# Optimization experiments

Measured on AMD Instinct MI355X. Metric: run time of the kernel, lower is better.

The kernel has to match this reference:

```python
import jax, jax.numpy as jnp
import numpy as np

NUM_HEADS = 8
CHUNK = 2
TAU = 2.0

# --- LIF neuron with ATan surrogate gradient (spikingjelly MultiStepLIFNode, hard reset to 0, detach_reset) ---
@jax.custom_vjp
def spike(x):
    return (x >= 0.0).astype(x.dtype)

def _spike_fwd(x):
    return spike(x), x

def _spike_bwd(x, g):
    alpha = 2.0
    sg = (alpha / 2.0) / (1.0 + (jnp.pi / 2.0 * alpha * x) ** 2)
    return (g * sg,)

spike.defvjp(_spike_fwd, _spike_bwd)

def lif(x_seq, v_th=1.0):
    # x_seq: [T, ...]; v' = v + (x - v)/tau ; spike if v' >= v_th ; hard reset v=0 (reset path detached)
    def step(v, x):
        v = v + (x - v) / TAU
        s = spike(v - v_th)
        v = v * (1.0 - jax.lax.stop_gradient(s))
        return v, s
    _, s = jax.lax.scan(step, jnp.zeros_like(x_seq[0]), x_seq)
    return s

def conv1x1_bn(x, W, scale, bias, conv_bias=None):
    # 1x1 conv over channel dim + eval-mode BN (per-channel affine)
    y = jnp.einsum('tbchw,dc->tbdhw', x, W)
    if conv_bias is not None:
        y = y + conv_bias[None, None, :, None, None]
    return y * scale[None, None, :, None, None] + bias[None, None, :, None, None]


def setup_inputs() -> dict:
    key = jax.random.key(0)
    ks = jax.random.split(key, 16)
    T, B, C, H, W = 4, 32, 512, 16, 16
    s = 1.0 / np.sqrt(C)
    return {
        'x': jax.random.normal(ks[0], (T, B, C, H, W), jnp.float32),
        'Wq': jax.random.normal(ks[1], (C, C), jnp.float32) * s,
        'q_scale': jax.random.uniform(ks[2], (C,), jnp.float32, 0.5, 1.5),
        'q_bias': jax.random.normal(ks[3], (C,), jnp.float32) * 0.1,
        'Wk': jax.random.normal(ks[4], (C, C), jnp.float32) * s,
        'k_scale': jax.random.uniform(ks[5], (C,), jnp.float32, 0.5, 1.5),
        'k_bias': jax.random.normal(ks[6], (C,), jnp.float32) * 0.1,
        'Wv': jax.random.normal(ks[7], (C, C), jnp.float32) * s,
        'v_scale': jax.random.uniform(ks[8], (C,), jnp.float32, 0.5, 1.5),
        'v_bias': jax.random.normal(ks[9], (C,), jnp.float32) * 0.1,
        'Wp': jax.random.normal(ks[10], (C, C), jnp.float32) * s,
        'bp': jax.random.normal(ks[11], (C,), jnp.float32) * 0.1,
        'p_scale': jax.random.uniform(ks[12], (C,), jnp.float32, 0.5, 1.5),
        'p_bias': jax.random.normal(ks[13], (C,), jnp.float32) * 0.1,
    }


def reference(x, Wq, q_scale, q_bias, Wk, k_scale, k_bias, Wv, v_scale, v_bias, Wp, bp, p_scale, p_bias):
    T, B, C, H, W = x.shape
    N = H * W
    hd = C // NUM_HEADS
    identity = x

    xs = lif(x)  # shortcut_lif

    def qkv_branch(W_, sc, bi):
        y = lif(conv1x1_bn(xs, W_, sc, bi))           # [T,B,C,H,W] spikes
        # flatten(3).transpose(-1,-2).reshape(...heads...).permute == split C, swap N/hd
        return jnp.swapaxes(y.reshape(T, B, NUM_HEADS, hd, N), -1, -2)  # [T,B,h,N,hd]

    q = qkv_branch(Wq, q_scale, q_bias)
    k = qkv_branch(Wk, k_scale, k_bias)
    v = qkv_branch(Wv, v_scale, v_bias)

    # STAtten: temporal chunking, linear attention q @ (k^T v)
    scaling = 1.0 / H
    nc = T // CHUNK

    def to_chunks(y):  # [T,B,h,N,hd] -> [nc,B,h,CHUNK*N,hd]
        return (y.reshape(nc, CHUNK, B, NUM_HEADS, N, hd)
                 .transpose(0, 2, 3, 1, 4, 5)
                 .reshape(nc, B, NUM_HEADS, CHUNK * N, hd))

    qc, kc, vc = to_chunks(q), to_chunks(k), to_chunks(v)
    attn = jnp.einsum('nbhsd,nbhse->nbhde', kc, vc) * scaling   # [nc,B,h,hd,hd]
    out = jnp.einsum('nbhsd,nbhde->nbhse', qc, attn)            # [nc,B,h,CHUNK*N,hd]
    out = (out.reshape(nc, B, NUM_HEADS, CHUNK, N, hd)
              .transpose(0, 3, 1, 2, 4, 5)
              .reshape(T, B, NUM_HEADS, N, hd))

    x2 = jnp.swapaxes(out, -1, -2).reshape(T, B, C, N)          # [T,B,C,N]
    x2 = lif(x2, v_th=0.5).reshape(T, B, C, H, W)               # attn_lif

    x3 = conv1x1_bn(x2, Wp, p_scale, p_bias, conv_bias=bp)      # proj conv+BN
    return x3 + identity, v
```

## Files before the change

### kernel.cpp

```cpp
#include <hip/hip_runtime.h>

typedef unsigned short ushort_t;
typedef unsigned char u8;
typedef short bf16x8 __attribute__((ext_vector_type(8)));
typedef float f32x4 __attribute__((ext_vector_type(4)));

#define T_DIM 4
#define B_DIM 32
#define C_DIM 512
#define N_DIM 256

__device__ __forceinline__ float bf2f(ushort_t u) {
  union { unsigned int i; float f; } x;
  x.i = ((unsigned int)u) << 16;
  return x.f;
}
__device__ __forceinline__ ushort_t f2bf(float f) {
  unsigned int u = __float_as_uint(f);
  u = (u + 0x7FFFu + ((u >> 16) & 1u)) >> 16;
  return (ushort_t)u;
}

__device__ __forceinline__ void gload16(const void* g, void* l) {
  __builtin_amdgcn_global_load_lds(
      (const __attribute__((address_space(1))) unsigned int*)g,
      (__attribute__((address_space(3))) unsigned int*)l, 16, 0, 0);
}

__device__ __forceinline__ unsigned int spike2bf(unsigned int w) {
  unsigned int r;
  asm("v_mul_u32_u24 %0, 0x3f80, %1" : "=v"(r) : "v"(w));
  return r;
}
__device__ __forceinline__ bf16x8 expand_spikes(uint2 raw) {
  union { bf16x8 v; unsigned int u[4]; } bu;
  bu.u[0] = spike2bf(__builtin_amdgcn_perm(0u, raw.x, 0x05010400u));
  bu.u[1] = spike2bf(__builtin_amdgcn_perm(0u, raw.x, 0x07030602u));
  bu.u[2] = spike2bf(__builtin_amdgcn_perm(0u, raw.y, 0x05010400u));
  bu.u[3] = spike2bf(__builtin_amdgcn_perm(0u, raw.y, 0x07030602u));
  return bu.v;
}

__global__ __launch_bounds__(256) void k0_split(
    const float* __restrict__ Wq, const float* __restrict__ Wk,
    const float* __restrict__ Wv, const float* __restrict__ Wp,
    ushort_t* __restrict__ Sqkv, ushort_t* __restrict__ Sp)
{
  int gid = blockIdx.x * 256 + threadIdx.x;
  int w = gid >> 15;
  int off = (gid & 32767) * 8;
  const float* src = (w == 0) ? Wq : ((w == 1) ? Wk : ((w == 2) ? Wv : Wp));
  ushort_t* dst = (w < 3) ? (Sqkv + (size_t)w * 3 * 262144) : Sp;
  float wv[8];
  *(float4*)&wv[0] = *(const float4*)(src + off);
  *(float4*)&wv[4] = *(const float4*)(src + off + 4);
  ushort_t hi[8], mi[8], lo[8];
#pragma unroll
  for (int i = 0; i < 8; i++) {
    float f = wv[i];
    ushort_t h = f2bf(f);  float r  = f - bf2f(h);
    ushort_t m = f2bf(r);  float r2 = r - bf2f(m);
    ushort_t l = f2bf(r2);
    hi[i] = h; mi[i] = m; lo[i] = l;
  }
  *(uint4*)(dst + off)              = *(uint4*)&hi[0];
  *(uint4*)(dst + 262144 + off)     = *(uint4*)&mi[0];
  *(uint4*)(dst + 2 * 262144 + off) = *(uint4*)&lo[0];
}

__global__ __launch_bounds__(256) void k1_shortcut_lif(
    const float* __restrict__ x, u8* __restrict__ xsT8)
{
  const int n0 = blockIdx.x * 64;
  const int c0 = blockIdx.y * 64;
  const int b  = blockIdx.z;
  __shared__ u8 sm[64][80];
  const int tid = threadIdx.x;
  const int r  = tid >> 2;
  const int j0 = (tid & 3) * 16;
  float v[16];
#pragma unroll
  for (int i = 0; i < 16; i++) v[i] = 0.f;
  for (int t = 0; t < T_DIM; t++) {
    const float* xp = x + ((((size_t)t * B_DIM + b) * C_DIM) + c0 + r) * N_DIM + n0 + j0;
    float xv[16];
    *(float4*)&xv[0]  = *(const float4*)xp;
    *(float4*)&xv[4]  = *(const float4*)(xp + 4);
    *(float4*)&xv[8]  = *(const float4*)(xp + 8);
    *(float4*)&xv[12] = *(const float4*)(xp + 12);
    __syncthreads();
#pragma unroll
    for (int i = 0; i < 16; i++) {
      float nv = v[i] + (xv[i] - v[i]) * 0.5f;
      bool s = (nv >= 1.0f);
      v[i] = s ? 0.f : nv;
      sm[j0 + i][r] = s ? (u8)1 : (u8)0;
    }
    __syncthreads();
    union { uint4 u; u8 b[16]; } ov;
#pragma unroll
    for (int i = 0; i < 16; i++) ov.b[i] = sm[r][j0 + i];
    u8* op = xsT8 + ((((size_t)t * B_DIM + b) * N_DIM) + n0 + r) * C_DIM + c0 + j0;
    *(uint4*)op = ov.u;
  }
}

__global__ __launch_bounds__(512, 4) void k2_qkv(
    const u8* __restrict__ xsT8, const ushort_t* __restrict__ Sqkv,
    const float* __restrict__ qsc, const float* __restrict__ qbi,
    const float* __restrict__ ksc, const float* __restrict__ kbi,
    const float* __restrict__ vsc, const float* __restrict__ vbi,
    u8* __restrict__ qs8T, u8* __restrict__ ks8, float* __restrict__ vout,
    u8* __restrict__ vs8T)
{
  const int lin = blockIdx.x + blockIdx.y * 24;
  const int b   = (lin & 7) | (((lin >> 3) & 3) << 3);
  const int mt  = lin >> 5;
  const int branch = mt >> 3;
  const int mloc = (mt & 7) * 64;
  const ushort_t* Ws = Sqkv + (size_t)branch * 3 * 262144;
  const float* scp = (branch == 0) ? qsc : ((branch == 1) ? ksc : vsc);
  const float* bip = (branch == 0) ? qbi : ((branch == 1) ? kbi : vbi);

  __shared__ alignas(16) ushort_t As[4][2][64][32];
  __shared__ alignas(16) u8 Bs8[4][256][32];

  const int tid  = threadIdx.x;
  const int lane = tid & 63;
  const int wave = tid >> 6;
  const int wm   = wave >> 2;
  const int wn   = wave & 3;
  const int frow = lane & 15;
  const int fsl  = lane >> 4;
  const int aswc = (fsl ^ ((frow >> 1) & 3)) * 8;
  const int bswc = (((fsl >> 1) ^ (((frow >> 2) ^ (frow >> 3)) & 1)) << 4)
                 + ((fsl & 1) << 3);

  const u8* Bb0 = xsT8 + (size_t)b * N_DIM * C_DIM;

  const int a0p = wave >> 2, a0q = wave & 3;
  const int arl = lane >> 2;
  const int acl = (((lane & 3) ^ ((arl >> 1) & 3)) * 8);
  const int brl = lane >> 1;
  const int bcl = (((lane & 1) ^ ((brl >> 2) & 1) ^ ((brl >> 3) & 1)) * 16);
  const int cbx = wave;

#define K2_STAGE(s_) {                                                                     \
    const int ss_ = (s_);                                                                  \
    const int t_ = ss_ >> 4; const int kb_ = (ss_ & 15) * 32; const int bf_ = ss_ & 3;     \
    gload16(Ws + (size_t)a0p * 262144 + (size_t)(mloc + a0q * 16 + arl) * 512 + kb_ + acl, \
            &As[bf_][a0p][a0q * 16][0]);                                                   \
    gload16(Bb0 + (size_t)t_ * (B_DIM * N_DIM * C_DIM) + (size_t)(cbx * 32 + brl) * 512 + kb_ + bcl, \
            &Bs8[bf_][cbx * 32][0]);                                                       \
  }

  f32x4 acc[8];
  float vst[32];
#pragma unroll
  for (int i = 0; i < 32; i++) vst[i] = 0.f;
#pragma unroll
  for (int j = 0; j < 8; j++) acc[j] = (f32x4){0.f, 0.f, 0.f, 0.f};

  const int crow0 = (lane >> 4) * 4;
  const int cn    = lane & 15;
  float sc8[2][4], bi8[2][4];
#pragma unroll
  for (int mi = 0; mi < 2; mi++)
#pragma unroll
    for (int r = 0; r < 4; r++) {
      int c = mloc + wm * 32 + mi * 16 + crow0 + r;
      sc8[mi][r] = scp[c]; bi8[mi][r] = bip[c];
    }

  K2_STAGE(0);
  K2_STAGE(1);

  for (int s = 0; s < 64; s++) {
    const int cur = s & 3;
    if (s < 62) K2_STAGE(s + 2);

    if (s < 62)       asm volatile("s_waitcnt vmcnt(4)" ::: "memory");
    else if (s == 62) asm volatile("s_waitcnt vmcnt(2)" ::: "memory");
    else              asm volatile("s_waitcnt vmcnt(0)" ::: "memory");
    __builtin_amdgcn_s_barrier();
    __builtin_amdgcn_sched_barrier(0);

    bf16x8 bfr[4];
#pragma unroll
    for (int nj = 0; nj < 4; nj++)
      bfr[nj] = expand_spikes(*(const uint2*)&Bs8[cur][wn * 64 + nj * 16 + frow][bswc]);

#pragma unroll
    for (int mi = 0; mi < 2; mi++) {
      const int ar = wm * 32 + mi * 16 + frow;
      bf16x8 a0 = *(const bf16x8*)&As[cur][0][ar][aswc];
      bf16x8 a1 = *(const bf16x8*)&As[cur][1][ar][aswc];
#pragma unroll
      for (int nj = 0; nj < 4; nj++) {
        acc[mi * 4 + nj] = __builtin_amdgcn_mfma_f32_16x16x32_bf16(a0, bfr[nj], acc[mi * 4 + nj], 0, 0, 0);
        acc[mi * 4 + nj] = __builtin_amdgcn_mfma_f32_16x16x32_bf16(a1, bfr[nj], acc[mi * 4 + nj], 0, 0, 0);
      }
    }

    if ((s & 15) == 15) {
      const int t = s >> 4;
      const size_t tb = (size_t)t * B_DIM + b;
      if (branch == 0) {
#pragma unroll
        for (int mi = 0; mi < 2; mi++) {
          const int c0 = mloc + wm * 32 + mi * 16 + crow0;
#pragma unroll
          for (int nj = 0; nj < 4; nj++) {
            const int n = wn * 64 + nj * 16 + cn;
            u8 sv[4];
#pragma unroll
            for (int r = 0; r < 4; r++) {
              float y = acc[mi * 4 + nj][r] * sc8[mi][r] + bi8[mi][r];
              const int vi = (mi * 4 + nj) * 4 + r;
              float v = vst[vi];
              v = v + (y - v) * 0.5f;
              bool sp = (v >= 1.0f);
              vst[vi] = sp ? 0.f : v;
              sv[r] = sp ? (u8)1 : (u8)0;
            }
            *(uchar4*)(qs8T + (tb * N_DIM + n) * C_DIM + c0) =
                make_uchar4(sv[0], sv[1], sv[2], sv[3]);
          }
        }
      } else if (branch == 1) {
#pragma unroll
        for (int mi = 0; mi < 2; mi++)
#pragma unroll
          for (int r = 0; r < 4; r++) {
            const int c = mloc + wm * 32 + mi * 16 + crow0 + r;
#pragma unroll
            for (int nj = 0; nj < 4; nj++) {
              const int n = wn * 64 + nj * 16 + cn;
              float y = acc[mi * 4 + nj][r] * sc8[mi][r] + bi8[mi][r];
              const int vi = (mi * 4 + nj) * 4 + r;
              float v = vst[vi];
              v = v + (y - v) * 0.5f;
              bool sp = (v >= 1.0f);
              vst[vi] = sp ? 0.f : v;
              ks8[(tb * C_DIM + c) * N_DIM + n] = sp ? (u8)1 : (u8)0;
            }
          }
      } else {
        const int hv = mloc >> 6;
#pragma unroll
        for (int mi = 0; mi < 2; mi++) {
          const int d0 = wm * 32 + mi * 16 + crow0;
#pragma unroll
          for (int nj = 0; nj < 4; nj++) {
            const int n = wn * 64 + nj * 16 + cn;
            float ov[4];
            u8 sv[4];
#pragma unroll
            for (int r = 0; r < 4; r++) {
              float y = acc[mi * 4 + nj][r] * sc8[mi][r] + bi8[mi][r];
              const int vi = (mi * 4 + nj) * 4 + r;
              float v = vst[vi];
              v = v + (y - v) * 0.5f;
              bool sp = (v >= 1.0f);
              vst[vi] = sp ? 0.f : v;
              ov[r] = sp ? 1.0f : 0.0f;
              sv[r] = sp ? (u8)1 : (u8)0;
            }
            *(float4*)(vout + ((tb * 8 + hv) * N_DIM + n) * 64 + d0) =
                make_float4(ov[0], ov[1], ov[2], ov[3]);
#pragma unroll
            for (int r = 0; r < 4; r++)
              vs8T[((tb * 8 + hv) * 64 + d0 + r) * N_DIM + n] = sv[r];
          }
        }
      }
#pragma unroll
      for (int j = 0; j < 8; j++) acc[j] = (f32x4){0.f, 0.f, 0.f, 0.f};
    }
  }
#undef K2_STAGE
}

__global__ __launch_bounds__(256) void k3_attn(
    const u8* __restrict__ ks8, const u8* __restrict__ vs8T,
    ushort_t* __restrict__ attnT2)
{
  const int h  = blockIdx.x;
  const int b  = blockIdx.y;
  const int ch = blockIdx.z;
  __shared__ alignas(16) u8 Ks[4][64][32];
  __shared__ alignas(16) u8 Vs[4][64][32];
  const int tid  = threadIdx.x;
  const int lane = tid & 63;
  const int wave = tid >> 6;
  const int wrow = wave * 16;
  const int frow = lane & 15;
  const int fsl  = lane >> 4;
  const int brl  = lane >> 1;
  const int bcl  = (((lane & 1) ^ ((brl >> 2) & 1) ^ ((brl >> 3) & 1)) * 16);

#define K3_STAGE(s_) {                                                                     \
    const int ss_ = (s_);                                                                  \
    const int t_ = ch * 2 + (ss_ >> 3); const int kb_ = (ss_ & 7) * 32; const int bf_ = ss_ & 3; \
    if (wave < 2)                                                                          \
      gload16(ks8 + ((((size_t)t_ * B_DIM + b) * C_DIM) + h * 64 + wave * 32 + brl) * N_DIM + kb_ + bcl, \
              &Ks[bf_][wave * 32][0]);                                                     \
    else                                                                                   \
      gload16(vs8T + ((((size_t)t_ * B_DIM + b) * 8 + h) * 64 + (wave - 2) * 32 + brl) * N_DIM + kb_ + bcl, \
              &Vs[bf_][(wave - 2) * 32][0]);                                               \
  }

  f32x4 acc[4];
#pragma unroll
  for (int i = 0; i < 4; i++) acc[i] = (f32x4){0.f, 0.f, 0.f, 0.f};

  K3_STAGE(0);
  K3_STAGE(1);

  for (int s = 0; s < 16; s++) {
    const int cur = s & 3;
    if (s < 14) K3_STAGE(s + 2);

    if (s < 14)       asm volatile("s_waitcnt vmcnt(2)" ::: "memory");
    else if (s == 14) asm volatile("s_waitcnt vmcnt(1)" ::: "memory");
    else              asm volatile("s_waitcnt vmcnt(0)" ::: "memory");
    __builtin_amdgcn_s_barrier();
    __builtin_amdgcn_sched_barrier(0);

    const int arow = wrow + frow;
    const int axx  = ((arow >> 2) ^ (arow >> 3)) & 1;
    const int asw  = (((fsl >> 1) ^ axx) << 4) + ((fsl & 1) << 3);
    bf16x8 af = expand_spikes(*(const uint2*)&Ks[cur][arow][asw]);

#pragma unroll
    for (int nt = 0; nt < 4; nt++) {
      const int row = nt * 16 + frow;
      const int bx  = ((row >> 2) ^ (row >> 3)) & 1;
      const int bsw = (((fsl >> 1) ^ bx) << 4) + ((fsl & 1) << 3);
      bf16x8 bv = expand_spikes(*(const uint2*)&Vs[cur][row][bsw]);
      acc[nt] = __builtin_amdgcn_mfma_f32_16x16x32_bf16(af, bv, acc[nt], 0, 0, 0);
    }
  }

  const int cn    = lane & 15;
  const int crow0 = (lane >> 4) * 4;
  const int d     = wrow + crow0;
  const int ks2   = d >> 5;
  const int dl    = d & 31;
  const size_t blk = ((size_t)(ch * B_DIM + b) * 8 + h);
#pragma unroll
  for (int nt = 0; nt < 4; nt++) {
    const int e = nt * 16 + cn;
    union { ushort_t sv[4]; uint2 u; } H, M;
#pragma unroll
    for (int r = 0; r < 4; r++) {
      float a = acc[nt][r] * 0.0625f;
      ushort_t hi = f2bf(a);
      float m = a - bf2f(hi);
      H.sv[r] = hi;
      M.sv[r] = f2bf(m);
    }
    *(uint2*)(attnT2 + ((blk * 2 + 0) * 2 + ks2) * 2048 + (size_t)e * 32 + dl) = H.u;
    *(uint2*)(attnT2 + ((blk * 2 + 1) * 2 + ks2) * 2048 + (size_t)e * 32 + dl) = M.u;
  }
#undef K3_STAGE
}

__global__ __launch_bounds__(256) void k4_out_lif(
    const u8* __restrict__ qs8T, const ushort_t* __restrict__ attnT2,
    u8* __restrict__ x2sT8)
{
  const int h  = blockIdx.x;
  const int b  = blockIdx.y;
  const int nc = blockIdx.z;
  __shared__ alignas(16) ushort_t As[2][2][2][64][32];
  __shared__ alignas(16) u8 Bs[2][128][32];
  const int tid  = threadIdx.x;
  const int lane = tid & 63;
  const int wave = tid >> 6;
  const int wrow = wave * 16;
  const int frow = lane & 15;
  const int fsl  = lane >> 4;
  const int arl  = lane >> 2;
  const int acl  = (((lane & 3) ^ ((arl >> 1) & 3)) * 8);
  const int brl  = lane >> 1;
  const int bcl  = (((lane & 1) ^ ((brl >> 2) & 1) ^ ((brl >> 3) & 1)) * 16);

#define K4_STAGEB(s_) {                                                                    \
    const int ss_ = (s_); const int t_ = ss_ >> 1; const int ks_ = ss_ & 1;                \
    gload16(qs8T + (((size_t)t_ * B_DIM + b) * N_DIM + nc * 128 + wave * 32 + brl) * C_DIM \
                 + h * 64 + ks_ * 32 + bcl,                                                \
            &Bs[ss_ & 1][wave * 32][0]);                                                   \
  }

#pragma unroll
  for (int i = 0; i < 8; i++) {
    const int c  = wave * 8 + i;
    const int chb = c >> 4, c4 = c & 15;
    const int p = c4 >> 3, ks = (c4 >> 2) & 1, g = c4 & 3;
    const size_t blk = ((size_t)(chb * B_DIM + b) * 8 + h);
    gload16(attnT2 + (((blk * 2 + p) * 2 + ks) * 64 + g * 16 + arl) * 32 + acl,
            &As[chb][p][ks][g * 16][0]);
  }
  K4_STAGEB(0);
  asm volatile("s_waitcnt vmcnt(0)" ::: "memory");
  __builtin_amdgcn_s_barrier();
  __builtin_amdgcn_sched_barrier(0);

  f32x4 acc[8];
  float vst[32];
#pragma unroll
  for (int i = 0; i < 32; i++) vst[i] = 0.f;

  const int cn    = lane & 15;
  const int crow0 = (lane >> 4) * 4;

  for (int sg = 0; sg < 8; sg++) {
    const int cur = sg & 1;
    if (sg < 7) K4_STAGEB(sg + 1);

    const int chb = sg >> 2, ks = sg & 1;
    if (ks == 0) {
#pragma unroll
      for (int j = 0; j < 8; j++) acc[j] = (f32x4){0.f, 0.f, 0.f, 0.f};
    }

    bf16x8 af[2];
    const int ar = wrow + frow;
    const int asw = (fsl ^ ((ar >> 1) & 3)) * 8;
#pragma unroll
    for (int p = 0; p < 2; p++) af[p] = *(const bf16x8*)&As[chb][p][ks][ar][asw];

#pragma unroll
    for (int j = 0; j < 8; j++) {
      const int row = j * 16 + frow;
      const int bx  = ((row >> 2) ^ (row >> 3)) & 1;
      const int bsw = (((fsl >> 1) ^ bx) << 4) + ((fsl & 1) << 3);
      bf16x8 bv = expand_spikes(*(const uint2*)&Bs[cur][row][bsw]);
#pragma unroll
      for (int p = 0; p < 2; p++)
        acc[j] = __builtin_amdgcn_mfma_f32_16x16x32_bf16(af[p], bv, acc[j], 0, 0, 0);
    }

    if (ks == 1) {
      const int t = sg >> 1;
      const size_t tb = (size_t)t * B_DIM + b;
#pragma unroll
      for (int j = 0; j < 8; j++) {
        const int n = nc * 128 + j * 16 + cn;
        u8 sv[4];
#pragma unroll
        for (int r = 0; r < 4; r++) {
          const int vi = j * 4 + r;
          float y = acc[j][r];
          float nv = vst[vi] + (y - vst[vi]) * 0.5f;
          bool sp = (nv >= 0.5f);
          vst[vi] = sp ? 0.f : nv;
          sv[r] = sp ? (u8)1 : (u8)0;
        }
        *(uchar4*)(x2sT8 + (tb * N_DIM + n) * C_DIM + h * 64 + wrow + crow0) =
            make_uchar4(sv[0], sv[1], sv[2], sv[3]);
      }
    }

    asm volatile("s_waitcnt vmcnt(0)" ::: "memory");
    __builtin_amdgcn_s_barrier();
    __builtin_amdgcn_sched_barrier(0);
  }
#undef K4_STAGEB
}

__global__ __launch_bounds__(512, 4) void k5_proj(
    const u8* __restrict__ x2sT8, const ushort_t* __restrict__ Sp,
    const float* __restrict__ bp, const float* __restrict__ psc,
    const float* __restrict__ pbi,
    const float* __restrict__ x, float* __restrict__ out0)
{
  const int tb = blockIdx.x;
  const int mt = blockIdx.y;
  const int mloc = mt * 64;

  __shared__ alignas(16) ushort_t As[4][2][64][32];
  __shared__ alignas(16) u8 Bs8[4][256][32];

  const int tid  = threadIdx.x;
  const int lane = tid & 63;
  const int wave = tid >> 6;
  const int wm   = wave >> 2;
  const int wn   = wave & 3;
  const int frow = lane & 15;
  const int fsl  = lane >> 4;
  const int aswc = (fsl ^ ((frow >> 1) & 3)) * 8;
  const int bswc = (((fsl >> 1) ^ (((frow >> 2) ^ (frow >> 3)) & 1)) << 4)
                 + ((fsl & 1) << 3);

  const u8* Bb = x2sT8 + (size_t)tb * N_DIM * C_DIM;

  const int a0p = wave >> 2, a0q = wave & 3;
  const int arl = lane >> 2;
  const int acl = (((lane & 3) ^ ((arl >> 1) & 3)) * 8);
  const int brl = lane >> 1;
  const int bcl = (((lane & 1) ^ ((brl >> 2) & 1) ^ ((brl >> 3) & 1)) * 16);
  const int cbx = wave;

#define K5_STAGE(s_) {                                                                     \
    const int ss_ = (s_); const int kb_ = ss_ * 32; const int bf_ = ss_ & 3;               \
    gload16(Sp + (size_t)a0p * 262144 + (size_t)(mloc + a0q * 16 + arl) * 512 + kb_ + acl, \
            &As[bf_][a0p][a0q * 16][0]);                                                   \
    gload16(Bb + (size_t)(cbx * 32 + brl) * 512 + kb_ + bcl, &Bs8[bf_][cbx * 32][0]);      \
  }

  f32x4 acc[8];
#pragma unroll
  for (int j = 0; j < 8; j++) acc[j] = (f32x4){0.f, 0.f, 0.f, 0.f};

  K5_STAGE(0);
  K5_STAGE(1);

  for (int s = 0; s < 16; s++) {
    const int cur = s & 3;
    if (s < 14) K5_STAGE(s + 2);

    if (s < 14)       asm volatile("s_waitcnt vmcnt(4)" ::: "memory");
    else if (s == 14) asm volatile("s_waitcnt vmcnt(2)" ::: "memory");
    else              asm volatile("s_waitcnt vmcnt(0)" ::: "memory");
    __builtin_amdgcn_s_barrier();
    __builtin_amdgcn_sched_barrier(0);

    bf16x8 bfr[4];
#pragma unroll
    for (int nj = 0; nj < 4; nj++)
      bfr[nj] = expand_spikes(*(const uint2*)&Bs8[cur][wn * 64 + nj * 16 + frow][bswc]);

#pragma unroll
    for (int mi = 0; mi < 2; mi++) {
      const int ar = wm * 32 + mi * 16 + frow;
      bf16x8 a0 = *(const bf16x8*)&As[cur][0][ar][aswc];
      bf16x8 a1 = *(const bf16x8*)&As[cur][1][ar][aswc];
#pragma unroll
      for (int nj = 0; nj < 4; nj++) {
        acc[mi * 4 + nj] = __builtin_amdgcn_mfma_f32_16x16x32_bf16(a0, bfr[nj], acc[mi * 4 + nj], 0, 0, 0);
        acc[mi * 4 + nj] = __builtin_amdgcn_mfma_f32_16x16x32_bf16(a1, bfr[nj], acc[mi * 4 + nj], 0, 0, 0);
      }
    }
  }

  const int crow0 = (lane >> 4) * 4;
  const int cn    = lane & 15;
#pragma unroll
  for (int mi = 0; mi < 2; mi++)
#pragma unroll
    for (int r = 0; r < 4; r++) {
      const int c = mloc + wm * 32 + mi * 16 + crow0 + r;
      const float scf = psc[c];
      const float bif = pbi[c];
      const float bpf = bp[c];
#pragma unroll
      for (int nj = 0; nj < 4; nj++) {
        const int n = wn * 64 + nj * 16 + cn;
        const size_t idx = ((size_t)tb * C_DIM + c) * N_DIM + n;
        out0[idx] = (acc[mi * 4 + nj][r] + bpf) * scf + bif + x[idx];
      }
    }
#undef K5_STAGE
}

extern "C" void kernel_launch(void* const* d_in, const int* in_sizes, int n_in,
                              void* d_out, int out_size, void* d_ws, size_t ws_size,
                              hipStream_t stream) {
  const float* x   = (const float*)d_in[0];
  const float* Wq  = (const float*)d_in[1];
  const float* qsc = (const float*)d_in[2];
  const float* qbi = (const float*)d_in[3];
  const float* Wk  = (const float*)d_in[4];
  const float* ksc = (const float*)d_in[5];
  const float* kbi = (const float*)d_in[6];
  const float* Wv  = (const float*)d_in[7];
  const float* vsc = (const float*)d_in[8];
  const float* vbi = (const float*)d_in[9];
  const float* Wp  = (const float*)d_in[10];
  const float* bp  = (const float*)d_in[11];
  const float* psc = (const float*)d_in[12];
  const float* pbi = (const float*)d_in[13];

  float* out0 = (float*)d_out;
  float* out1 = out0 + 16777216;

  const size_t M16 = 16u * 1024u * 1024u;
  char* o0 = (char*)d_out;
  char* ws = (char*)d_ws;

  u8*       xsT8   = (u8*)(o0);
  ushort_t* attnT2 = (ushort_t*)(o0);
  u8*       qs8T   = (u8*)(o0 + M16);
  u8*       ks8    = (u8*)(o0 + 2 * M16);
  u8*       vs8T   = (u8*)(o0 + 3 * M16);
  u8*       x2sT8  = (u8*)(ws);
  ushort_t* Sqkv   = (ushort_t*)(ws);
  ushort_t* Sp     = (ushort_t*)(ws + M16);

  hipLaunchKernelGGL(k0_split,        dim3(512),        dim3(256), 0, stream,
                     Wq, Wk, Wv, Wp, Sqkv, Sp);
  hipLaunchKernelGGL(k1_shortcut_lif, dim3(4, 8, 32),   dim3(256), 0, stream, x, xsT8);
  hipLaunchKernelGGL(k2_qkv,          dim3(24, 32),     dim3(512), 0, stream,
                     xsT8, Sqkv, qsc, qbi, ksc, kbi, vsc, vbi, qs8T, ks8, out1, vs8T);
  hipLaunchKernelGGL(k3_attn,         dim3(8, 32, 2),   dim3(256), 0, stream,
                     ks8, vs8T, attnT2);
  hipLaunchKernelGGL(k4_out_lif,      dim3(8, 32, 2),   dim3(256), 0, stream,
                     qs8T, attnT2, x2sT8);
  hipLaunchKernelGGL(k5_proj,         dim3(128, 8),     dim3(512), 0, stream,
                     x2sT8, Sp, bp, psc, pbi, x, out0);
}
```

Baseline: 431.2 us.

## Replace bf16 split-weight MFMA with two-level int8 weights and i8 MFMA

Weights are quantized per output row into two int8 levels (a coarse value plus a scaled residual) instead of a three-way bf16 split. The QKV, projection and attention GEMMs then use int8 MFMA directly on the 0/1 spike bytes. This removes the spike-to-bf16 expansion, halves the A-operand bytes and shared-memory footprint, and uses the higher-throughput int8 MFMA path. The cost is precision: the two-level int8 weights are less accurate than the three-term bf16 split, so results near spike thresholds may differ slightly from the reference.

```diff
diff --git a/kernel.cpp b/kernel.cpp
--- a/kernel.cpp
+++ b/kernel.cpp
@@ -4,6 +4,7 @@
 typedef unsigned char u8;
 typedef short bf16x8 __attribute__((ext_vector_type(8)));
 typedef float f32x4 __attribute__((ext_vector_type(4)));
+typedef int i32x4 __attribute__((ext_vector_type(4)));
 
 #define T_DIM 4
 #define B_DIM 32
@@ -41,31 +42,45 @@
   return bu.v;
 }
 
-__global__ __launch_bounds__(256) void k0_split(
+__global__ __launch_bounds__(256) void k0_quant_i8(
     const float* __restrict__ Wq, const float* __restrict__ Wk,
     const float* __restrict__ Wv, const float* __restrict__ Wp,
-    ushort_t* __restrict__ Sqkv, ushort_t* __restrict__ Sp)
+    u8* __restrict__ SqkvI8, u8* __restrict__ SpI8,
+    float* __restrict__ sQKV, float* __restrict__ sP)
 {
-  int gid = blockIdx.x * 256 + threadIdx.x;
-  int w = gid >> 15;
-  int off = (gid & 32767) * 8;
-  const float* src = (w == 0) ? Wq : ((w == 1) ? Wk : ((w == 2) ? Wv : Wp));
-  ushort_t* dst = (w < 3) ? (Sqkv + (size_t)w * 3 * 262144) : Sp;
+  const int w = threadIdx.x >> 6;
+  const int l = threadIdx.x & 63;
+  const int row = blockIdx.x * 4 + w;
+  const int m = row >> 9;
+  const int c = row & 511;
+  const float* src = (m == 0) ? Wq : ((m == 1) ? Wk : ((m == 2) ? Wv : Wp));
   float wv[8];
-  *(float4*)&wv[0] = *(const float4*)(src + off);
-  *(float4*)&wv[4] = *(const float4*)(src + off + 4);
-  ushort_t hi[8], mi[8], lo[8];
+  *(float4*)&wv[0] = *(const float4*)(src + (size_t)c * 512 + l * 8);
+  *(float4*)&wv[4] = *(const float4*)(src + (size_t)c * 512 + l * 8 + 4);
+  float mx = 0.f;
+#pragma unroll
+  for (int i = 0; i < 8; i++) mx = fmaxf(mx, fabsf(wv[i]));
+#pragma unroll
+  for (int off = 1; off < 64; off <<= 1) mx = fmaxf(mx, __shfl_xor(mx, off));
+  const float s1   = mx * (1.0f / 127.0f);
+  const float inv1 = (mx > 0.f) ? 127.0f / mx : 0.f;
+  const float inv2 = inv1 * 254.0f;
+  union { char cc[8]; uint2 u; } Q1, Q2;
 #pragma unroll
   for (int i = 0; i < 8; i++) {
-    float f = wv[i];
-    ushort_t h = f2bf(f);  float r  = f - bf2f(h);
-    ushort_t m = f2bf(r);  float r2 = r - bf2f(m);
-    ushort_t l = f2bf(r2);
-    hi[i] = h; mi[i] = m; lo[i] = l;
-  }
-  *(uint4*)(dst + off)              = *(uint4*)&hi[0];
-  *(uint4*)(dst + 262144 + off)     = *(uint4*)&mi[0];
-  *(uint4*)(dst + 2 * 262144 + off) = *(uint4*)&lo[0];
+    int a = __float2int_rn(wv[i] * inv1);
+    a = (a > 127) ? 127 : ((a < -127) ? -127 : a);
+    float r = wv[i] - s1 * (float)a;
+    int b2 = __float2int_rn(r * inv2);
+    b2 = (b2 > 127) ? 127 : ((b2 < -127) ? -127 : b2);
+    Q1.cc[i] = (char)a; Q2.cc[i] = (char)b2;
+  }
+  u8* dst = (m < 3) ? (SqkvI8 + (size_t)m * 2 * 262144) : SpI8;
+  *(uint2*)(dst + (size_t)c * 512 + l * 8)          = Q1.u;
+  *(uint2*)(dst + 262144 + (size_t)c * 512 + l * 8) = Q2.u;
+  if (l == 0) {
+    if (m < 3) sQKV[m * 512 + c] = s1; else sP[c] = s1;
+  }
 }
 
 __global__ __launch_bounds__(256) void k1_shortcut_lif(
@@ -106,7 +121,8 @@
 }
 
 __global__ __launch_bounds__(512, 4) void k2_qkv(
-    const u8* __restrict__ xsT8, const ushort_t* __restrict__ Sqkv,
+    const u8* __restrict__ xsT8, const u8* __restrict__ SqkvI8,
+    const float* __restrict__ sQKV,
     const float* __restrict__ qsc, const float* __restrict__ qbi,
     const float* __restrict__ ksc, const float* __restrict__ kbi,
     const float* __restrict__ vsc, const float* __restrict__ vbi,
@@ -118,11 +134,12 @@
   const int mt  = lin >> 5;
   const int branch = mt >> 3;
   const int mloc = (mt & 7) * 64;
-  const ushort_t* Ws = Sqkv + (size_t)branch * 3 * 262144;
+  const u8* Wi8 = SqkvI8 + (size_t)branch * 2 * 262144;
+  const float* s1p = sQKV + branch * 512;
   const float* scp = (branch == 0) ? qsc : ((branch == 1) ? ksc : vsc);
   const float* bip = (branch == 0) ? qbi : ((branch == 1) ? kbi : vbi);
 
-  __shared__ alignas(16) ushort_t As[4][2][64][32];
+  __shared__ alignas(16) u8 As8[4][2][64][32];
   __shared__ alignas(16) u8 Bs8[4][256][32];
 
   const int tid  = threadIdx.x;
@@ -132,44 +149,43 @@
   const int wn   = wave & 3;
   const int frow = lane & 15;
   const int fsl  = lane >> 4;
-  const int aswc = (fsl ^ ((frow >> 1) & 3)) * 8;
-  const int bswc = (((fsl >> 1) ^ (((frow >> 2) ^ (frow >> 3)) & 1)) << 4)
-                 + ((fsl & 1) << 3);
+  const int off8 = (fsl ^ (((frow >> 3) & 1) << 1)) * 8;
+  const int hsw  = (((lane & 1) ^ ((lane >> 4) & 1)) * 16);
+  const int srow = lane >> 1;
 
   const u8* Bb0 = xsT8 + (size_t)b * N_DIM * C_DIM;
-
-  const int a0p = wave >> 2, a0q = wave & 3;
-  const int arl = lane >> 2;
-  const int acl = (((lane & 3) ^ ((arl >> 1) & 3)) * 8);
-  const int brl = lane >> 1;
-  const int bcl = (((lane & 1) ^ ((brl >> 2) & 1) ^ ((brl >> 3) & 1)) * 16);
-  const int cbx = wave;
 
 #define K2_STAGE(s_) {                                                                     \
     const int ss_ = (s_);                                                                  \
     const int t_ = ss_ >> 4; const int kb_ = (ss_ & 15) * 32; const int bf_ = ss_ & 3;     \
-    gload16(Ws + (size_t)a0p * 262144 + (size_t)(mloc + a0q * 16 + arl) * 512 + kb_ + acl, \
-            &As[bf_][a0p][a0q * 16][0]);                                                   \
-    gload16(Bb0 + (size_t)t_ * (B_DIM * N_DIM * C_DIM) + (size_t)(cbx * 32 + brl) * 512 + kb_ + bcl, \
-            &Bs8[bf_][cbx * 32][0]);                                                       \
-  }
-
-  f32x4 acc[8];
+    if (wave < 4)                                                                          \
+      gload16(Wi8 + (size_t)(wave >> 1) * 262144 +                                         \
+              (size_t)(mloc + (wave & 1) * 32 + srow) * 512 + kb_ + hsw,                   \
+              &As8[bf_][wave >> 1][(wave & 1) * 32][0]);                                   \
+    gload16(Bb0 + (size_t)t_ * (B_DIM * N_DIM * C_DIM) +                                   \
+            (size_t)(wave * 32 + srow) * 512 + kb_ + hsw,                                  \
+            &Bs8[bf_][wave * 32][0]);                                                      \
+  }
+
+  i32x4 accA[8], accB[8];
   float vst[32];
 #pragma unroll
   for (int i = 0; i < 32; i++) vst[i] = 0.f;
 #pragma unroll
-  for (int j = 0; j < 8; j++) acc[j] = (f32x4){0.f, 0.f, 0.f, 0.f};
+  for (int j = 0; j < 8; j++) { accA[j] = (i32x4){0,0,0,0}; accB[j] = (i32x4){0,0,0,0}; }
 
   const int crow0 = (lane >> 4) * 4;
   const int cn    = lane & 15;
-  float sc8[2][4], bi8[2][4];
+  float G1[2][4], G2[2][4], bi8[2][4];
 #pragma unroll
   for (int mi = 0; mi < 2; mi++)
 #pragma unroll
     for (int r = 0; r < 4; r++) {
       int c = mloc + wm * 32 + mi * 16 + crow0 + r;
-      sc8[mi][r] = scp[c]; bi8[mi][r] = bip[c];
+      float s1 = s1p[c], sc = scp[c];
+      G1[mi][r] = s1 * sc;
+      G2[mi][r] = s1 * (1.0f / 254.0f) * sc;
+      bi8[mi][r] = bip[c];
     }
 
   K2_STAGE(0);
@@ -179,26 +195,32 @@
     const int cur = s & 3;
     if (s < 62) K2_STAGE(s + 2);
 
-    if (s < 62)       asm volatile("s_waitcnt vmcnt(4)" ::: "memory");
-    else if (s == 62) asm volatile("s_waitcnt vmcnt(2)" ::: "memory");
-    else              asm volatile("s_waitcnt vmcnt(0)" ::: "memory");
+    if (s < 62) {
+      if (wave < 4) asm volatile("s_waitcnt vmcnt(4)" ::: "memory");
+      else          asm volatile("s_waitcnt vmcnt(2)" ::: "memory");
+    } else if (s == 62) {
+      if (wave < 4) asm volatile("s_waitcnt vmcnt(2)" ::: "memory");
+      else          asm volatile("s_waitcnt vmcnt(1)" ::: "memory");
+    } else {
+      asm volatile("s_waitcnt vmcnt(0)" ::: "memory");
+    }
     __builtin_amdgcn_s_barrier();
     __builtin_amdgcn_sched_barrier(0);
 
-    bf16x8 bfr[4];
+    long bl[4];
 #pragma unroll
     for (int nj = 0; nj < 4; nj++)
-      bfr[nj] = expand_spikes(*(const uint2*)&Bs8[cur][wn * 64 + nj * 16 + frow][bswc]);
+      bl[nj] = *(const long*)&Bs8[cur][wn * 64 + nj * 16 + frow][off8];
 
 #pragma unroll
     for (int mi = 0; mi < 2; mi++) {
       const int ar = wm * 32 + mi * 16 + frow;
-      bf16x8 a0 = *(const bf16x8*)&As[cur][0][ar][aswc];
-      bf16x8 a1 = *(const bf16x8*)&As[cur][1][ar][aswc];
+      const long p0 = *(const long*)&As8[cur][0][ar][off8];
+      const long p1 = *(const long*)&As8[cur][1][ar][off8];
 #pragma unroll
       for (int nj = 0; nj < 4; nj++) {
-        acc[mi * 4 + nj] = __builtin_amdgcn_mfma_f32_16x16x32_bf16(a0, bfr[nj], acc[mi * 4 + nj], 0, 0, 0);
-        acc[mi * 4 + nj] = __builtin_amdgcn_mfma_f32_16x16x32_bf16(a1, bfr[nj], acc[mi * 4 + nj], 0, 0, 0);
+        accA[mi * 4 + nj] = __builtin_amdgcn_mfma_i32_16x16x32_i8(p0, bl[nj], accA[mi * 4 + nj], 0, 0, 0);
+        accB[mi * 4 + nj] = __builtin_amdgcn_mfma_i32_16x16x32_i8(p1, bl[nj], accB[mi * 4 + nj], 0, 0, 0);
       }
     }
 
@@ -215,7 +237,8 @@
             u8 sv[4];
 #pragma unroll
             for (int r = 0; r < 4; r++) {
-              float y = acc[mi * 4 + nj][r] * sc8[mi][r] + bi8[mi][r];
+              float y = (float)accA[mi * 4 + nj][r] * G1[mi][r]
+                      + (float)accB[mi * 4 + nj][r] * G2[mi][r] + bi8[mi][r];
               const int vi = (mi * 4 + nj) * 4 + r;
               float v = vst[vi];
               v = v + (y - v) * 0.5f;
@@ -236,7 +259,8 @@
 #pragma unroll
             for (int nj = 0; nj < 4; nj++) {
               const int n = wn * 64 + nj * 16 + cn;
-              float y = acc[mi * 4 + nj][r] * sc8[mi][r] + bi8[mi][r];
+              float y = (float)accA[mi * 4 + nj][r] * G1[mi][r]
+                      + (float)accB[mi * 4 + nj][r] * G2[mi][r] + bi8[mi][r];
               const int vi = (mi * 4 + nj) * 4 + r;
               float v = vst[vi];
               v = v + (y - v) * 0.5f;
@@ -257,7 +281,8 @@
             u8 sv[4];
 #pragma unroll
             for (int r = 0; r < 4; r++) {
-              float y = acc[mi * 4 + nj][r] * sc8[mi][r] + bi8[mi][r];
+              float y = (float)accA[mi * 4 + nj][r] * G1[mi][r]
+                      + (float)accB[mi * 4 + nj][r] * G2[mi][r] + bi8[mi][r];
               const int vi = (mi * 4 + nj) * 4 + r;
               float v = vst[vi];
               v = v + (y - v) * 0.5f;
@@ -275,7 +300,7 @@
         }
       }
 #pragma unroll
-      for (int j = 0; j < 8; j++) acc[j] = (f32x4){0.f, 0.f, 0.f, 0.f};
+      for (int j = 0; j < 8; j++) { accA[j] = (i32x4){0,0,0,0}; accB[j] = (i32x4){0,0,0,0}; }
     }
   }
 #undef K2_STAGE
@@ -293,26 +318,26 @@
   const int tid  = threadIdx.x;
   const int lane = tid & 63;
   const int wave = tid >> 6;
-  const int wrow = wave * 16;
   const int frow = lane & 15;
   const int fsl  = lane >> 4;
-  const int brl  = lane >> 1;
-  const int bcl  = (((lane & 1) ^ ((brl >> 2) & 1) ^ ((brl >> 3) & 1)) * 16);
+  const int off8 = (fsl ^ (((frow >> 3) & 1) << 1)) * 8;
+  const int hsw  = (((lane & 1) ^ ((lane >> 4) & 1)) * 16);
+  const int srow = lane >> 1;
 
 #define K3_STAGE(s_) {                                                                     \
     const int ss_ = (s_);                                                                  \
     const int t_ = ch * 2 + (ss_ >> 3); const int kb_ = (ss_ & 7) * 32; const int bf_ = ss_ & 3; \
     if (wave < 2)                                                                          \
-      gload16(ks8 + ((((size_t)t_ * B_DIM + b) * C_DIM) + h * 64 + wave * 32 + brl) * N_DIM + kb_ + bcl, \
+      gload16(ks8 + ((((size_t)t_ * B_DIM + b) * C_DIM) + h * 64 + wave * 32 + srow) * N_DIM + kb_ + hsw, \
               &Ks[bf_][wave * 32][0]);                                                     \
     else                                                                                   \
-      gload16(vs8T + ((((size_t)t_ * B_DIM + b) * 8 + h) * 64 + (wave - 2) * 32 + brl) * N_DIM + kb_ + bcl, \
+      gload16(vs8T + ((((size_t)t_ * B_DIM + b) * 8 + h) * 64 + (wave - 2) * 32 + srow) * N_DIM + kb_ + hsw, \
               &Vs[bf_][(wave - 2) * 32][0]);                                               \
   }
 
-  f32x4 acc[4];
-#pragma unroll
-  for (int i = 0; i < 4; i++) acc[i] = (f32x4){0.f, 0.f, 0.f, 0.f};
+  i32x4 acc[4];
+#pragma unroll
+  for (int i = 0; i < 4; i++) acc[i] = (i32x4){0,0,0,0};
 
   K3_STAGE(0);
   K3_STAGE(1);
@@ -327,24 +352,17 @@
     __builtin_amdgcn_s_barrier();
     __builtin_amdgcn_sched_barrier(0);
 
-    const int arow = wrow + frow;
-    const int axx  = ((arow >> 2) ^ (arow >> 3)) & 1;
-    const int asw  = (((fsl >> 1) ^ axx) << 4) + ((fsl & 1) << 3);
-    bf16x8 af = expand_spikes(*(const uint2*)&Ks[cur][arow][asw]);
-
+    const long aK = *(const long*)&Ks[cur][wave * 16 + frow][off8];
 #pragma unroll
     for (int nt = 0; nt < 4; nt++) {
-      const int row = nt * 16 + frow;
-      const int bx  = ((row >> 2) ^ (row >> 3)) & 1;
-      const int bsw = (((fsl >> 1) ^ bx) << 4) + ((fsl & 1) << 3);
-      bf16x8 bv = expand_spikes(*(const uint2*)&Vs[cur][row][bsw]);
-      acc[nt] = __builtin_amdgcn_mfma_f32_16x16x32_bf16(af, bv, acc[nt], 0, 0, 0);
+      const long bV = *(const long*)&Vs[cur][nt * 16 + frow][off8];
+      acc[nt] = __builtin_amdgcn_mfma_i32_16x16x32_i8(aK, bV, acc[nt], 0, 0, 0);
     }
   }
 
   const int cn    = lane & 15;
   const int crow0 = (lane >> 4) * 4;
-  const int d     = wrow + crow0;
+  const int d     = wave * 16 + crow0;
   const int ks2   = d >> 5;
   const int dl    = d & 31;
   const size_t blk = ((size_t)(ch * B_DIM + b) * 8 + h);
@@ -354,7 +372,7 @@
     union { ushort_t sv[4]; uint2 u; } H, M;
 #pragma unroll
     for (int r = 0; r < 4; r++) {
-      float a = acc[nt][r] * 0.0625f;
+      float a = (float)acc[nt][r] * 0.0625f;
       ushort_t hi = f2bf(a);
       float m = a - bf2f(hi);
       H.sv[r] = hi;
@@ -471,7 +489,8 @@
 }
 
 __global__ __launch_bounds__(512, 4) void k5_proj(
-    const u8* __restrict__ x2sT8, const ushort_t* __restrict__ Sp,
+    const u8* __restrict__ x2sT8, const u8* __restrict__ SpI8,
+    const float* __restrict__ sP,
     const float* __restrict__ bp, const float* __restrict__ psc,
     const float* __restrict__ pbi,
     const float* __restrict__ x, float* __restrict__ out0)
@@ -480,7 +499,7 @@
   const int mt = blockIdx.y;
   const int mloc = mt * 64;
 
-  __shared__ alignas(16) ushort_t As[4][2][64][32];
+  __shared__ alignas(16) u8 As8[4][2][64][32];
   __shared__ alignas(16) u8 Bs8[4][256][32];
 
   const int tid  = threadIdx.x;
@@ -490,29 +509,24 @@
   const int wn   = wave & 3;
   const int frow = lane & 15;
   const int fsl  = lane >> 4;
-  const int aswc = (fsl ^ ((frow >> 1) & 3)) * 8;
-  const int bswc = (((fsl >> 1) ^ (((frow >> 2) ^ (frow >> 3)) & 1)) << 4)
-                 + ((fsl & 1) << 3);
+  const int off8 = (fsl ^ (((frow >> 3) & 1) << 1)) * 8;
+  const int hsw  = (((lane & 1) ^ ((lane >> 4) & 1)) * 16);
+  const int srow = lane >> 1;
 
   const u8* Bb = x2sT8 + (size_t)tb * N_DIM * C_DIM;
-
-  const int a0p = wave >> 2, a0q = wave & 3;
-  const int arl = lane >> 2;
-  const int acl = (((lane & 3) ^ ((arl >> 1) & 3)) * 8);
-  const int brl = lane >> 1;
-  const int bcl = (((lane & 1) ^ ((brl >> 2) & 1) ^ ((brl >> 3) & 1)) * 16);
-  const int cbx = wave;
 
 #define K5_STAGE(s_) {                                                                     \
     const int ss_ = (s_); const int kb_ = ss_ * 32; const int bf_ = ss_ & 3;               \
-    gload16(Sp + (size_t)a0p * 262144 + (size_t)(mloc + a0q * 16 + arl) * 512 + kb_ + acl, \
-            &As[bf_][a0p][a0q * 16][0]);                                                   \
-    gload16(Bb + (size_t)(cbx * 32 + brl) * 512 + kb_ + bcl, &Bs8[bf_][cbx * 32][0]);      \
-  }
-
-  f32x4 acc[8];
-#pragma unroll
-  for (int j = 0; j < 8; j++) acc[j] = (f32x4){0.f, 0.f, 0.f, 0.f};
+    if (wave < 4)                                                                          \
+      gload16(SpI8 + (size_t)(wave >> 1) * 262144 +                                        \
+              (size_t)(mloc + (wave & 1) * 32 + srow) * 512 + kb_ + hsw,                   \
+              &As8[bf_][wave >> 1][(wave & 1) * 32][0]);                                   \
+    gload16(Bb + (size_t)(wave * 32 + srow) * 512 + kb_ + hsw, &Bs8[bf_][wave * 32][0]);   \
+  }
+
+  i32x4 accA[8], accB[8];
+#pragma unroll
+  for (int j = 0; j < 8; j++) { accA[j] = (i32x4){0,0,0,0}; accB[j] = (i32x4){0,0,0,0}; }
 
   K5_STAGE(0);
   K5_STAGE(1);
@@ -521,26 +535,32 @@
     const int cur = s & 3;
     if (s < 14) K5_STAGE(s + 2);
 
-    if (s < 14)       asm volatile("s_waitcnt vmcnt(4)" ::: "memory");
-    else if (s == 14) asm volatile("s_waitcnt vmcnt(2)" ::: "memory");
-    else              asm volatile("s_waitcnt vmcnt(0)" ::: "memory");
+    if (s < 14) {
+      if (wave < 4) asm volatile("s_waitcnt vmcnt(4)" ::: "memory");
+      else          asm volatile("s_waitcnt vmcnt(2)" ::: "memory");
+    } else if (s == 14) {
+      if (wave < 4) asm volatile("s_waitcnt vmcnt(2)" ::: "memory");
+      else          asm volatile("s_waitcnt vmcnt(1)" ::: "memory");
+    } else {
+      asm volatile("s_waitcnt vmcnt(0)" ::: "memory");
+    }
     __builtin_amdgcn_s_barrier();
     __builtin_amdgcn_sched_barrier(0);
 
-    bf16x8 bfr[4];
+    long bl[4];
 #pragma unroll
     for (int nj = 0; nj < 4; nj++)
-      bfr[nj] = expand_spikes(*(const uint2*)&Bs8[cur][wn * 64 + nj * 16 + frow][bswc]);
+      bl[nj] = *(const long*)&Bs8[cur][wn * 64 + nj * 16 + frow][off8];
 
 #pragma unroll
     for (int mi = 0; mi < 2; mi++) {
       const int ar = wm * 32 + mi * 16 + frow;
-      bf16x8 a0 = *(const bf16x8*)&As[cur][0][ar][aswc];
-      bf16x8 a1 = *(const bf16x8*)&As[cur][1][ar][aswc];
+      const long p0 = *(const long*)&As8[cur][0][ar][off8];
+      const long p1 = *(const long*)&As8[cur][1][ar][off8];
 #pragma unroll
       for (int nj = 0; nj < 4; nj++) {
-        acc[mi * 4 + nj] = __builtin_amdgcn_mfma_f32_16x16x32_bf16(a0, bfr[nj], acc[mi * 4 + nj], 0, 0, 0);
-        acc[mi * 4 + nj] = __builtin_amdgcn_mfma_f32_16x16x32_bf16(a1, bfr[nj], acc[mi * 4 + nj], 0, 0, 0);
+        accA[mi * 4 + nj] = __builtin_amdgcn_mfma_i32_16x16x32_i8(p0, bl[nj], accA[mi * 4 + nj], 0, 0, 0);
+        accB[mi * 4 + nj] = __builtin_amdgcn_mfma_i32_16x16x32_i8(p1, bl[nj], accB[mi * 4 + nj], 0, 0, 0);
       }
     }
   }
@@ -552,14 +572,17 @@
 #pragma unroll
     for (int r = 0; r < 4; r++) {
       const int c = mloc + wm * 32 + mi * 16 + crow0 + r;
+      const float s1 = sP[c];
       const float scf = psc[c];
-      const float bif = pbi[c];
-      const float bpf = bp[c];
+      const float g1 = s1 * scf;
+      const float g2 = s1 * (1.0f / 254.0f) * scf;
+      const float b0 = bp[c] * scf + pbi[c];
 #pragma unroll
       for (int nj = 0; nj < 4; nj++) {
         const int n = wn * 64 + nj * 16 + cn;
         const size_t idx = ((size_t)tb * C_DIM + c) * N_DIM + n;
-        out0[idx] = (acc[mi * 4 + nj][r] + bpf) * scf + bif + x[idx];
+        out0[idx] = (float)accA[mi * 4 + nj][r] * g1
+                  + (float)accB[mi * 4 + nj][r] * g2 + b0 + x[idx];
       }
     }
 #undef K5_STAGE
@@ -596,18 +619,21 @@
   u8*       ks8    = (u8*)(o0 + 2 * M16);
   u8*       vs8T   = (u8*)(o0 + 3 * M16);
   u8*       x2sT8  = (u8*)(ws);
-  ushort_t* Sqkv   = (ushort_t*)(ws);
-  ushort_t* Sp     = (ushort_t*)(ws + M16);
-
-  hipLaunchKernelGGL(k0_split,        dim3(512),        dim3(256), 0, stream,
-                     Wq, Wk, Wv, Wp, Sqkv, Sp);
+  u8*       SqkvI8 = (u8*)(ws);
+  float*    sQKV   = (float*)(ws + 3 * 2 * 262144);
+  u8*       SpI8   = (u8*)(ws + M16);
+  float*    sP     = (float*)(ws + M16 + 2 * 262144);
+
+  hipLaunchKernelGGL(k0_quant_i8,     dim3(512),        dim3(256), 0, stream,
+                     Wq, Wk, Wv, Wp, SqkvI8, SpI8, sQKV, sP);
   hipLaunchKernelGGL(k1_shortcut_lif, dim3(4, 8, 32),   dim3(256), 0, stream, x, xsT8);
   hipLaunchKernelGGL(k2_qkv,          dim3(24, 32),     dim3(512), 0, stream,
-                     xsT8, Sqkv, qsc, qbi, ksc, kbi, vsc, vbi, qs8T, ks8, out1, vs8T);
+                     xsT8, SqkvI8, sQKV, qsc, qbi, ksc, kbi, vsc, vbi,
+                     qs8T, ks8, out1, vs8T);
   hipLaunchKernelGGL(k3_attn,         dim3(8, 32, 2),   dim3(256), 0, stream,
                      ks8, vs8T, attnT2);
   hipLaunchKernelGGL(k4_out_lif,      dim3(8, 32, 2),   dim3(256), 0, stream,
                      qs8T, attnT2, x2sT8);
   hipLaunchKernelGGL(k5_proj,         dim3(128, 8),     dim3(512), 0, stream,
-                     x2sT8, Sp, bp, psc, pbi, x, out0);
-}
+                     x2sT8, SpI8, sP, bp, psc, pbi, x, out0);
+}
```

Measured after the change: 518.5 us. +20.2%, slower.
